# Kernel optimization log

Hardware: AMD Instinct MI355X
Metric: run time of the kernel (lower is better)

The kernel has to match this reference:

```python
import jax, jax.numpy as jnp
import numpy as np

B, S, SIZE = 2048, 512, 96  # size = embedding_size(32) * num_feature(3)


def setup_inputs() -> dict:
    key = jax.random.key(0)
    k1, k2, k3, k4, k5, k6, k7 = jax.random.split(key, 7)
    bound = 1.0 / np.sqrt(SIZE)  # nn.Linear default init range
    return {
        "seq_item_embedding": jax.random.normal(k1, (B, S, SIZE), dtype=jnp.float32),
        "target_item_embedding": jax.random.normal(k2, (B, 1, SIZE), dtype=jnp.float32),
        "mask": jax.random.randint(k3, (B, S + 1, 1), 0, 2).astype(jnp.bool_),
        "w1_weight": jax.random.uniform(k4, (SIZE, SIZE), jnp.float32, -bound, bound),
        "w1_bias": jax.random.uniform(k5, (SIZE,), jnp.float32, -bound, bound),
        "w2_weight": jax.random.uniform(k6, (SIZE, SIZE), jnp.float32, -bound, bound),
        "w2_bias": jax.random.uniform(k7, (SIZE,), jnp.float32, -bound, bound),
    }


def reference(seq_item_embedding, target_item_embedding, mask,
              w1_weight, w1_bias, w2_weight, w2_bias):
    # mask[:, :-1, :] -> [B, S] boolean (True = masked out)
    m = mask[:, :-1, 0]
    # w1(seq): [B, S, size]; note source reassigns seq_item_embedding to this,
    # so the final weighted pool uses the projected sequence.
    seq_h = jnp.einsum('bsd,ed->bse', seq_item_embedding, w1_weight) + w1_bias
    # w2(target): [B, 1, size], broadcasts over seq_len (repeat in torch)
    tgt_h = jnp.einsum('bqd,ed->bqe', target_item_embedding, w2_weight) + w2_bias
    # sigmoid(sum) reduced over feature dim -> scores [B, S]
    scores = jax.nn.sigmoid(seq_h + tgt_h).sum(axis=-1)
    scores = jnp.where(m, jnp.float32(-1e9), scores)
    attn = jax.nn.softmax(scores, axis=-1)  # [B, S]
    # weighted pool over seq dim -> [B, size]
    output = jnp.einsum('bs,bse->be', attn, seq_h)
    return output
```

## Files before the change

### kernel.cpp

```cpp
#include <hip/hip_runtime.h>
#include <math.h>

#define NB 2048
#define NS 512
#define ND 96

typedef __attribute__((ext_vector_type(8))) short short8;
typedef __attribute__((ext_vector_type(4))) float floatx4;

__device__ __forceinline__ float sigm(float x) {
    return 1.0f / (1.0f + __expf(-x));
}
__device__ __forceinline__ short8 cvt8(floatx4 p0, floatx4 p1) {
    union { unsigned u[4]; short8 s; } r;
    asm("v_cvt_pk_bf16_f32 %0, %1, %2" : "=v"(r.u[0]) : "v"(p0[0]), "v"(p0[1]));
    asm("v_cvt_pk_bf16_f32 %0, %1, %2" : "=v"(r.u[1]) : "v"(p0[2]), "v"(p0[3]));
    asm("v_cvt_pk_bf16_f32 %0, %1, %2" : "=v"(r.u[2]) : "v"(p1[0]), "v"(p1[1]));
    asm("v_cvt_pk_bf16_f32 %0, %1, %2" : "=v"(r.u[3]) : "v"(p1[2]), "v"(p1[3]));
    return r.s;
}

__global__ __launch_bounds__(256, 4)
void attn_fused(const float* __restrict__ seq,
                const float* __restrict__ tgt,
                const int*   __restrict__ mask,
                const float* __restrict__ w1,
                const float* __restrict__ b1,
                const float* __restrict__ w2,
                const float* __restrict__ b2,
                float* __restrict__ out)
{
    __shared__ short w1f[18 * 64 * 8];
    __shared__ float thp2[ND][2];
    __shared__ float maskf[NS];
    __shared__ float red2[4];
    __shared__ float osum[4][ND];

    const int b    = blockIdx.x;
    const int tid  = threadIdx.x;
    const int lane = tid & 63;
    const int wave = tid >> 6;
    const int l15  = lane & 15;
    const int quad = lane >> 4;

    maskf[tid]       = (mask[(size_t)b * (NS + 1) + tid]       != 0) ? 0.0f : 1.0f;
    maskf[tid + 256] = (mask[(size_t)b * (NS + 1) + tid + 256] != 0) ? 0.0f : 1.0f;

    for (int idx = tid; idx < 1152; idx += 256) {
        const int e  = idx / 12;
        const int dc = idx - 12 * e;
        const int kk = dc >> 2;
        const int q  = dc & 3;
        const float* p = w1 + e * ND + kk * 32 + q * 8;
        floatx4 p0 = *(const floatx4*)(p);
        floatx4 p1 = *(const floatx4*)(p + 4);
        const int t = e >> 4, r = e & 15;
        *(short8*)&w1f[(((t * 3 + kk) * 64) + q * 16 + r) * 8] = cvt8(p0, p1);
    }

    if (tid < 2 * ND) {
        const int e    = tid >> 1;
        const int part = tid & 1;
        const float* tv = tgt + (size_t)b * ND + part * 48;
        const float* wr = w2 + e * ND + part * 48;
        float acc = 0.f;
        #pragma unroll
        for (int d = 0; d < 48; d += 4) {
            floatx4 a = *(const floatx4*)(tv + d);
            floatx4 w = *(const floatx4*)(wr + d);
            acc += a[0]*w[0] + a[1]*w[1] + a[2]*w[2] + a[3]*w[3];
        }
        thp2[e][part] = acc;
    }
    __syncthreads();

    float tgtv[6], biasv[6];
    #pragma unroll
    for (int t = 0; t < 6; ++t) {
        const int e = 16 * t + l15;
        tgtv[t]  = b2[e] + thp2[e][0] + thp2[e][1];
        biasv[t] = b1[e];
    }

    const float* abase = seq + ((size_t)b * NS + l15) * ND + quad * 8;
    float o_acc[6] = {0.f, 0.f, 0.f, 0.f, 0.f, 0.f};
    float sacc = 0.f;

    #pragma unroll 2
    for (int sti = 0; sti < 8; ++sti) {
        const int s0 = (wave * 8 + sti) * 16;
        short8 af[3];
        #pragma unroll
        for (int kk = 0; kk < 3; ++kk) {
            const float* p = abase + (size_t)s0 * ND + kk * 32;
            af[kk] = cvt8(*(const floatx4*)(p), *(const floatx4*)(p + 4));
        }
        floatx4 acc6[6];
        float p0s = 0.f, p1s = 0.f, p2s = 0.f, p3s = 0.f;
        #pragma unroll
        for (int t = 0; t < 6; ++t) {
            floatx4 acc = { biasv[t], biasv[t], biasv[t], biasv[t] };
            #pragma unroll
            for (int kk = 0; kk < 3; ++kk) {
                const short8 bf = *(const short8*)&w1f[((t * 3 + kk) * 64 + lane) * 8];
                acc = __builtin_amdgcn_mfma_f32_16x16x32_bf16(af[kk], bf, acc, 0, 0, 0);
            }
            acc6[t] = acc;
            const float thv = tgtv[t];
            p0s += sigm(acc[0] + thv);
            p1s += sigm(acc[1] + thv);
            p2s += sigm(acc[2] + thv);
            p3s += sigm(acc[3] + thv);
        }
        #pragma unroll
        for (int off = 1; off < 16; off <<= 1) {
            p0s += __shfl_xor(p0s, off, 64);
            p1s += __shfl_xor(p1s, off, 64);
            p2s += __shfl_xor(p2s, off, 64);
            p3s += __shfl_xor(p3s, off, 64);
        }
        const int sq = s0 + quad * 4;
        const float e0 = maskf[sq + 0] * __expf(p0s - 48.f);
        const float e1 = maskf[sq + 1] * __expf(p1s - 48.f);
        const float e2 = maskf[sq + 2] * __expf(p2s - 48.f);
        const float e3 = maskf[sq + 3] * __expf(p3s - 48.f);
        sacc += e0 + e1 + e2 + e3;
        #pragma unroll
        for (int t = 0; t < 6; ++t) {
            o_acc[t] += e0 * acc6[t][0] + e1 * acc6[t][1]
                      + e2 * acc6[t][2] + e3 * acc6[t][3];
        }
    }

    float ss = sacc;
    ss += __shfl_xor(ss, 16, 64);
    ss += __shfl_xor(ss, 32, 64);
    if (lane == 0) red2[wave] = ss;

    #pragma unroll
    for (int t = 0; t < 6; ++t) {
        o_acc[t] += __shfl_xor(o_acc[t], 16, 64);
        o_acc[t] += __shfl_xor(o_acc[t], 32, 64);
    }
    if (quad == 0) {
        #pragma unroll
        for (int t = 0; t < 6; ++t) osum[wave][16 * t + l15] = o_acc[t];
    }
    __syncthreads();
    if (tid < ND) {
        const float tot = red2[0] + red2[1] + red2[2] + red2[3];
        float a = 0.f;
        #pragma unroll
        for (int w = 0; w < 4; ++w) a += osum[w][tid];
        out[(size_t)b * ND + tid] = a * (1.0f / tot);
    }
}

extern "C" void kernel_launch(void* const* d_in, const int* in_sizes, int n_in,
                              void* d_out, int out_size, void* d_ws, size_t ws_size,
                              hipStream_t stream) {
    const float* seq  = (const float*)d_in[0];
    const float* tgt  = (const float*)d_in[1];
    const int*   mask = (const int*)d_in[2];
    const float* w1   = (const float*)d_in[3];
    const float* b1   = (const float*)d_in[4];
    const float* w2   = (const float*)d_in[5];
    const float* b2   = (const float*)d_in[6];
    float* out = (float*)d_out;
    attn_fused<<<dim3(NB), dim3(256), 0, stream>>>(seq, tgt, mask, w1, b1, w2, b2, out);
}
```

Measured before the change: 583.6 us.

## Recompute projection MFMAs instead of holding them, raising occupancy to 8 waves

Stops keeping the six projected accumulator tiles live across the softmax step. The MFMA projection is now recomputed after the scores are known, which cuts register pressure so launch bounds can request 8 blocks per CU and the loop unroll drops to 1. The mask is read directly from global memory per tile instead of staged in shared memory, and the target projection is simplified to one thread per output. The trade is twice the MFMA work and LDS weight reads in exchange for higher occupancy and better latency hiding of the sequence loads.

```diff
diff --git a/kernel.cpp b/kernel.cpp
--- a/kernel.cpp
+++ b/kernel.cpp
@@ -20,7 +20,7 @@
     return r.s;
 }
 
-__global__ __launch_bounds__(256, 4)
+__global__ __launch_bounds__(256, 8)
 void attn_fused(const float* __restrict__ seq,
                 const float* __restrict__ tgt,
                 const int*   __restrict__ mask,
@@ -31,8 +31,7 @@
                 float* __restrict__ out)
 {
     __shared__ short w1f[18 * 64 * 8];
-    __shared__ float thp2[ND][2];
-    __shared__ float maskf[NS];
+    __shared__ float th[ND];
     __shared__ float red2[4];
     __shared__ float osum[4][ND];
 
@@ -42,9 +41,6 @@
     const int wave = tid >> 6;
     const int l15  = lane & 15;
     const int quad = lane >> 4;
-
-    maskf[tid]       = (mask[(size_t)b * (NS + 1) + tid]       != 0) ? 0.0f : 1.0f;
-    maskf[tid + 256] = (mask[(size_t)b * (NS + 1) + tid + 256] != 0) ? 0.0f : 1.0f;
 
     for (int idx = tid; idx < 1152; idx += 256) {
         const int e  = idx / 12;
@@ -58,19 +54,20 @@
         *(short8*)&w1f[(((t * 3 + kk) * 64) + q * 16 + r) * 8] = cvt8(p0, p1);
     }
 
-    if (tid < 2 * ND) {
-        const int e    = tid >> 1;
-        const int part = tid & 1;
-        const float* tv = tgt + (size_t)b * ND + part * 48;
-        const float* wr = w2 + e * ND + part * 48;
-        float acc = 0.f;
+    if (tid < ND) {
+        const float* tv = tgt + (size_t)b * ND;
+        const float* wr = w2 + tid * ND;
+        float a0 = 0.f, a1 = 0.f;
         #pragma unroll
-        for (int d = 0; d < 48; d += 4) {
-            floatx4 a = *(const floatx4*)(tv + d);
-            floatx4 w = *(const floatx4*)(wr + d);
-            acc += a[0]*w[0] + a[1]*w[1] + a[2]*w[2] + a[3]*w[3];
+        for (int d = 0; d < ND; d += 8) {
+            floatx4 x0 = *(const floatx4*)(tv + d);
+            floatx4 w0 = *(const floatx4*)(wr + d);
+            floatx4 x1 = *(const floatx4*)(tv + d + 4);
+            floatx4 w1v = *(const floatx4*)(wr + d + 4);
+            a0 += x0[0]*w0[0] + x0[1]*w0[1] + x0[2]*w0[2] + x0[3]*w0[3];
+            a1 += x1[0]*w1v[0] + x1[1]*w1v[1] + x1[2]*w1v[2] + x1[3]*w1v[3];
         }
-        thp2[e][part] = acc;
+        th[tid] = b2[tid] + a0 + a1;
     }
     __syncthreads();
 
@@ -78,24 +75,29 @@
     #pragma unroll
     for (int t = 0; t < 6; ++t) {
         const int e = 16 * t + l15;
-        tgtv[t]  = b2[e] + thp2[e][0] + thp2[e][1];
+        tgtv[t]  = th[e];
         biasv[t] = b1[e];
     }
 
     const float* abase = seq + ((size_t)b * NS + l15) * ND + quad * 8;
+    const int*   mbase = mask + (size_t)b * (NS + 1) + quad * 4;
     float o_acc[6] = {0.f, 0.f, 0.f, 0.f, 0.f, 0.f};
     float sacc = 0.f;
 
-    #pragma unroll 2
+    #pragma unroll 1
     for (int sti = 0; sti < 8; ++sti) {
         const int s0 = (wave * 8 + sti) * 16;
-        short8 af[3];
+        union { short8 s; unsigned u[4]; } afu[3];
         #pragma unroll
         for (int kk = 0; kk < 3; ++kk) {
             const float* p = abase + (size_t)s0 * ND + kk * 32;
-            af[kk] = cvt8(*(const floatx4*)(p), *(const floatx4*)(p + 4));
+            afu[kk].s = cvt8(*(const floatx4*)(p), *(const floatx4*)(p + 4));
         }
-        floatx4 acc6[6];
+        const int mk0 = mbase[s0 + 0];
+        const int mk1 = mbase[s0 + 1];
+        const int mk2 = mbase[s0 + 2];
+        const int mk3 = mbase[s0 + 3];
+
         float p0s = 0.f, p1s = 0.f, p2s = 0.f, p3s = 0.f;
         #pragma unroll
         for (int t = 0; t < 6; ++t) {
@@ -103,9 +105,8 @@
             #pragma unroll
             for (int kk = 0; kk < 3; ++kk) {
                 const short8 bf = *(const short8*)&w1f[((t * 3 + kk) * 64 + lane) * 8];
-                acc = __builtin_amdgcn_mfma_f32_16x16x32_bf16(af[kk], bf, acc, 0, 0, 0);
+                acc = __builtin_amdgcn_mfma_f32_16x16x32_bf16(afu[kk].s, bf, acc, 0, 0, 0);
             }
-            acc6[t] = acc;
             const float thv = tgtv[t];
             p0s += sigm(acc[0] + thv);
             p1s += sigm(acc[1] + thv);
@@ -119,16 +120,27 @@
             p2s += __shfl_xor(p2s, off, 64);
             p3s += __shfl_xor(p3s, off, 64);
         }
-        const int sq = s0 + quad * 4;
-        const float e0 = maskf[sq + 0] * __expf(p0s - 48.f);
-        const float e1 = maskf[sq + 1] * __expf(p1s - 48.f);
-        const float e2 = maskf[sq + 2] * __expf(p2s - 48.f);
-        const float e3 = maskf[sq + 3] * __expf(p3s - 48.f);
+        const float e0 = (mk0 != 0) ? 0.f : __expf(p0s - 48.f);
+        const float e1 = (mk1 != 0) ? 0.f : __expf(p1s - 48.f);
+        const float e2 = (mk2 != 0) ? 0.f : __expf(p2s - 48.f);
+        const float e3 = (mk3 != 0) ? 0.f : __expf(p3s - 48.f);
         sacc += e0 + e1 + e2 + e3;
+
+        #pragma unroll
+        for (int kk = 0; kk < 3; ++kk) {
+            asm volatile("" : "+v"(afu[kk].u[0]), "+v"(afu[kk].u[1]),
+                              "+v"(afu[kk].u[2]), "+v"(afu[kk].u[3]));
+        }
+
         #pragma unroll
         for (int t = 0; t < 6; ++t) {
-            o_acc[t] += e0 * acc6[t][0] + e1 * acc6[t][1]
-                      + e2 * acc6[t][2] + e3 * acc6[t][3];
+            floatx4 acc = { biasv[t], biasv[t], biasv[t], biasv[t] };
+            #pragma unroll
+            for (int kk = 0; kk < 3; ++kk) {
+                const short8 bf = *(const short8*)&w1f[((t * 3 + kk) * 64 + lane) * 8];
+                acc = __builtin_amdgcn_mfma_f32_16x16x32_bf16(afu[kk].s, bf, acc, 0, 0, 0);
+            }
+            o_acc[t] += e0 * acc[0] + e1 * acc[1] + e2 * acc[2] + e3 * acc[3];
         }
     }
 
```

New measurement: 630.8 us. +8.1%, slower.
